# Performance work log

Hardware: AMD Instinct MI355X
Metric: run time of the kernel (lower is better)

The kernel has to match this reference:

```python
import jax, jax.numpy as jnp
import numpy as np

D_IN = 200   # 4 * d_embeddings
H = 64       # hidden_size

def setup_inputs() -> dict:
    key = jax.random.key(0)
    ks = jax.random.split(key, 7)
    B, T = 4096, 128
    s_ih = 1.0 / np.sqrt(H)
    x = jax.random.normal(ks[0], (B, T, D_IN), dtype=jnp.float32)
    W_ih = jax.random.uniform(ks[1], (H, D_IN), minval=-s_ih, maxval=s_ih, dtype=jnp.float32)
    W_hh = jax.random.uniform(ks[2], (H, H), minval=-s_ih, maxval=s_ih, dtype=jnp.float32)
    b_ih = jax.random.uniform(ks[3], (H,), minval=-s_ih, maxval=s_ih, dtype=jnp.float32)
    b_hh = jax.random.uniform(ks[4], (H,), minval=-s_ih, maxval=s_ih, dtype=jnp.float32)
    W_out = jax.random.uniform(ks[5], (1, H), minval=-s_ih, maxval=s_ih, dtype=jnp.float32)
    b_out = jax.random.uniform(ks[6], (1,), minval=-s_ih, maxval=s_ih, dtype=jnp.float32)
    return {"x": x, "W_ih": W_ih, "W_hh": W_hh, "b_ih": b_ih, "b_hh": b_hh,
            "W_out": W_out, "b_out": b_out}

def reference(x, W_ih, W_hh, b_ih, b_hh, W_out, b_out):
    B = x.shape[0]
    # precompute input projection for all timesteps: [B, T, H]
    xp = jnp.einsum('btd,hd->bth', x, W_ih) + b_ih + b_hh
    def step(h, xt):
        h = jnp.tanh(xt + h @ W_hh.T)
        return h, None
    h0 = jnp.zeros((B, H), dtype=x.dtype)
    h_last, _ = jax.lax.scan(step, h0, jnp.swapaxes(xp, 0, 1))  # scan over time
    return jax.nn.sigmoid(h_last @ W_out.T + b_out)  # [B, 1]
```

## Files before the change

### kernel.cpp

```cpp
#include <hip/hip_runtime.h>
#include <hip/hip_bf16.h>


#define TSEQ 128
#define DIN  200
#define HID  64
#define CT   16
#define NCH  (TSEQ/CT)

typedef short bf16x8 __attribute__((ext_vector_type(8)));
typedef float f32x4  __attribute__((ext_vector_type(4)));

__device__ __forceinline__ unsigned short f2bf(float f) {
  __hip_bfloat16 h = __float2bfloat16(f);
  return __builtin_bit_cast(unsigned short, h);
}
__device__ __forceinline__ bf16x8 cvt8(f32x4 a, f32x4 b) {
  bf16x8 r;
#pragma unroll
  for (int i = 0; i < 4; ++i) { r[i] = (short)f2bf(a[i]); r[4 + i] = (short)f2bf(b[i]); }
  return r;
}
__device__ __forceinline__ float tanh_fast(float x) {
  float e = exp2f(x * 2.885390081777927f);
  float r = __builtin_amdgcn_rcpf(1.f + e);
  return __builtin_fmaf(-2.f, r, 1.f);
}

__global__ __launch_bounds__(256, 3) void rnn_fused(
    const float* __restrict__ x,   const float* __restrict__ Wih,
    const float* __restrict__ Whh, const float* __restrict__ bih,
    const float* __restrict__ bhh, const float* __restrict__ Wout,
    const float* __restrict__ bout, float* __restrict__ out)
{
  __shared__ unsigned short wihL[28][64][8];
  __shared__ unsigned short hb[4][2][80];

  const int tid  = threadIdx.x;
  const int w    = tid >> 6;
  const int lane = tid & 63;
  const int m    = lane & 15;
  const int g    = lane >> 4;
  const int row  = blockIdx.x * 4 + w;

  const float* xl = x + ((size_t)row * TSEQ + m) * DIN;

  f32x4 px[7][2];
  auto LOADC = [&](int c) {
    const float* p = xl + (size_t)c * (CT * DIN);
#pragma unroll
    for (int ks = 0; ks < 6; ++ks) {
      const int d = ks * 32 + g * 8;
      px[ks][0] = *reinterpret_cast<const f32x4*>(p + d);
      px[ks][1] = *reinterpret_cast<const f32x4*>(p + d + 4);
    }
    px[6][0] = *reinterpret_cast<const f32x4*>(p + 192);
    px[6][1] = *reinterpret_cast<const f32x4*>(p + 196);
  };
  LOADC(0);

  for (int f = w; f < 28; f += 4) {
    const int nt = f / 7, ks = f % 7;
    const int d  = ks * 32 + g * 8;
    bf16x8 v = (bf16x8)0;
    if (d + 8 <= DIN) {
      const float* wr = Wih + (size_t)(nt * 16 + m) * DIN + d;
      v = cvt8(*reinterpret_cast<const f32x4*>(wr), *reinterpret_cast<const f32x4*>(wr + 4));
    }
    *reinterpret_cast<bf16x8*>(&wihL[f][lane][0]) = v;
  }

  bf16x8 whhf[4][2];
#pragma unroll
  for (int nt = 0; nt < 4; ++nt)
#pragma unroll
    for (int hf = 0; hf < 2; ++hf) {
      const float* wr = Whh + (size_t)(nt * 16 + m) * HID + hf * 32 + g * 8;
      whhf[nt][hf] = cvt8(*reinterpret_cast<const f32x4*>(wr),
                          *reinterpret_cast<const f32x4*>(wr + 4));
    }
  float biasv[4], woutv[4];
#pragma unroll
  for (int nt = 0; nt < 4; ++nt) {
    biasv[nt] = bih[nt * 16 + m] + bhh[nt * 16 + m];
    woutv[nt] = Wout[nt * 16 + m];
  }
  const float bout0 = bout[0];

  hb[w][0][lane] = 0;
  hb[w][1][lane] = 0;
  __syncthreads();

  float vfin[4] = {0.f, 0.f, 0.f, 0.f};

  for (int c = 0; c < NCH; ++c) {
    bf16x8 afr[7];
#pragma unroll
    for (int ks = 0; ks < 6; ++ks) afr[ks] = cvt8(px[ks][0], px[ks][1]);
    afr[6] = (g == 0) ? cvt8(px[6][0], px[6][1]) : (bf16x8)0;

    f32x4 acc[4];
#pragma unroll
    for (int nt = 0; nt < 4; ++nt) acc[nt] = (f32x4)(biasv[nt]);
#pragma unroll
    for (int ks = 0; ks < 7; ++ks) {
#pragma unroll
      for (int nt = 0; nt < 4; ++nt) {
        bf16x8 bv = *reinterpret_cast<const bf16x8*>(&wihL[nt * 7 + ks][lane][0]);
        acc[nt] = __builtin_amdgcn_mfma_f32_16x16x32_bf16(afr[ks], bv, acc[nt], 0, 0, 0);
      }
    }

    if (c + 1 < NCH) LOADC(c + 1);

#pragma unroll
    for (int s = 0; s < CT; ++s) {
      const int rb = s & 1, pb = rb ^ 1;
      asm volatile("" ::: "memory");
      bf16x8 ha0 = *reinterpret_cast<const bf16x8*>(&hb[w][pb][g * 8]);
      bf16x8 ha1 = *reinterpret_cast<const bf16x8*>(&hb[w][pb][32 + g * 8]);
      f32x4 racc[4];
#pragma unroll
      for (int nt = 0; nt < 4; ++nt)
        racc[nt] = __builtin_amdgcn_mfma_f32_16x16x32_bf16(ha0, whhf[nt][0], acc[nt], 0, 0, 0);
#pragma unroll
      for (int nt = 0; nt < 4; ++nt)
        racc[nt] = __builtin_amdgcn_mfma_f32_16x16x32_bf16(ha1, whhf[nt][1], racc[nt], 0, 0, 0);
      if (g == (s >> 2)) {
#pragma unroll
        for (int nt = 0; nt < 4; ++nt) {
          const float v = tanh_fast(racc[nt][s & 3]);
          hb[w][rb][nt * 16 + m] = f2bf(v);
          if (s == CT - 1) vfin[nt] = v;
        }
      }
      asm volatile("" ::: "memory");
    }
  }

  float sred = vfin[0] * woutv[0] + vfin[1] * woutv[1]
             + vfin[2] * woutv[2] + vfin[3] * woutv[3];
  sred += __shfl_xor(sred, 1, 64);
  sred += __shfl_xor(sred, 2, 64);
  sred += __shfl_xor(sred, 4, 64);
  sred += __shfl_xor(sred, 8, 64);
  if (lane == 48)
    out[row] = __builtin_amdgcn_rcpf(1.f + exp2f(-(sred + bout0) * 1.4426950408889634f));
}

extern "C" void kernel_launch(void* const* d_in, const int* in_sizes, int n_in,
                              void* d_out, int out_size, void* d_ws, size_t ws_size,
                              hipStream_t stream) {
  const float* x    = (const float*)d_in[0];
  const float* Wih  = (const float*)d_in[1];
  const float* Whh  = (const float*)d_in[2];
  const float* bih  = (const float*)d_in[3];
  const float* bhh  = (const float*)d_in[4];
  const float* Wout = (const float*)d_in[5];
  const float* bout = (const float*)d_in[6];
  float* out = (float*)d_out;

  const int B = in_sizes[0] / (TSEQ * DIN);
  rnn_fused<<<dim3(B / 4), dim3(256), 0, stream>>>(x, Wih, Whh, bih, bhh, Wout, bout, out);
}
```

Baseline: 117.1 us.

## Split x prefetch into two halves to cut registers and raise occupancy to 4

Launch bounds go from 3 to 4 waves per SIMD. To fit the tighter register budget, the full-chunk x prefetch register array is split in two. The first four k-slices are prefetched one chunk ahead, while the last three are loaded at the start of the current chunk. Wout and bout are now read at the end of the kernel instead of being held in registers. More resident waves should hide latency better, but half of the x loads are no longer overlapped with the recurrence, and spills can happen if the budget is still exceeded.

```diff
diff --git a/kernel.cpp b/kernel.cpp
--- a/kernel.cpp
+++ b/kernel.cpp
@@ -27,7 +27,7 @@
   return __builtin_fmaf(-2.f, r, 1.f);
 }
 
-__global__ __launch_bounds__(256, 3) void rnn_fused(
+__global__ __launch_bounds__(256, 4) void rnn_fused(
     const float* __restrict__ x,   const float* __restrict__ Wih,
     const float* __restrict__ Whh, const float* __restrict__ bih,
     const float* __restrict__ bhh, const float* __restrict__ Wout,
@@ -45,19 +45,28 @@
 
   const float* xl = x + ((size_t)row * TSEQ + m) * DIN;
 
-  f32x4 px[7][2];
-  auto LOADC = [&](int c) {
+  f32x4 pA[4][2], pB[3][2];
+  auto LOADA = [&](int c) {
     const float* p = xl + (size_t)c * (CT * DIN);
 #pragma unroll
-    for (int ks = 0; ks < 6; ++ks) {
+    for (int ks = 0; ks < 4; ++ks) {
       const int d = ks * 32 + g * 8;
-      px[ks][0] = *reinterpret_cast<const f32x4*>(p + d);
-      px[ks][1] = *reinterpret_cast<const f32x4*>(p + d + 4);
+      pA[ks][0] = *reinterpret_cast<const f32x4*>(p + d);
+      pA[ks][1] = *reinterpret_cast<const f32x4*>(p + d + 4);
     }
-    px[6][0] = *reinterpret_cast<const f32x4*>(p + 192);
-    px[6][1] = *reinterpret_cast<const f32x4*>(p + 196);
   };
-  LOADC(0);
+  auto LOADB = [&](int c) {
+    const float* p = xl + (size_t)c * (CT * DIN);
+#pragma unroll
+    for (int ks = 4; ks < 6; ++ks) {
+      const int d = ks * 32 + g * 8;
+      pB[ks - 4][0] = *reinterpret_cast<const f32x4*>(p + d);
+      pB[ks - 4][1] = *reinterpret_cast<const f32x4*>(p + d + 4);
+    }
+    pB[2][0] = *reinterpret_cast<const f32x4*>(p + 192);
+    pB[2][1] = *reinterpret_cast<const f32x4*>(p + 196);
+  };
+  LOADA(0);
 
   for (int f = w; f < 28; f += 4) {
     const int nt = f / 7, ks = f % 7;
@@ -79,13 +88,9 @@
       whhf[nt][hf] = cvt8(*reinterpret_cast<const f32x4*>(wr),
                           *reinterpret_cast<const f32x4*>(wr + 4));
     }
-  float biasv[4], woutv[4];
+  float biasv[4];
 #pragma unroll
-  for (int nt = 0; nt < 4; ++nt) {
-    biasv[nt] = bih[nt * 16 + m] + bhh[nt * 16 + m];
-    woutv[nt] = Wout[nt * 16 + m];
-  }
-  const float bout0 = bout[0];
+  for (int nt = 0; nt < 4; ++nt) biasv[nt] = bih[nt * 16 + m] + bhh[nt * 16 + m];
 
   hb[w][0][lane] = 0;
   hb[w][1][lane] = 0;
@@ -94,24 +99,31 @@
   float vfin[4] = {0.f, 0.f, 0.f, 0.f};
 
   for (int c = 0; c < NCH; ++c) {
-    bf16x8 afr[7];
-#pragma unroll
-    for (int ks = 0; ks < 6; ++ks) afr[ks] = cvt8(px[ks][0], px[ks][1]);
-    afr[6] = (g == 0) ? cvt8(px[6][0], px[6][1]) : (bf16x8)0;
+    LOADB(c);
 
     f32x4 acc[4];
 #pragma unroll
     for (int nt = 0; nt < 4; ++nt) acc[nt] = (f32x4)(biasv[nt]);
 #pragma unroll
-    for (int ks = 0; ks < 7; ++ks) {
+    for (int ks = 0; ks < 4; ++ks) {
+      const bf16x8 a = cvt8(pA[ks][0], pA[ks][1]);
 #pragma unroll
       for (int nt = 0; nt < 4; ++nt) {
         bf16x8 bv = *reinterpret_cast<const bf16x8*>(&wihL[nt * 7 + ks][lane][0]);
-        acc[nt] = __builtin_amdgcn_mfma_f32_16x16x32_bf16(afr[ks], bv, acc[nt], 0, 0, 0);
+        acc[nt] = __builtin_amdgcn_mfma_f32_16x16x32_bf16(a, bv, acc[nt], 0, 0, 0);
       }
     }
-
-    if (c + 1 < NCH) LOADC(c + 1);
+    if (c + 1 < NCH) LOADA(c + 1);
+#pragma unroll
+    for (int ks = 4; ks < 7; ++ks) {
+      const bf16x8 a = (ks < 6) ? cvt8(pB[ks - 4][0], pB[ks - 4][1])
+                                : ((g == 0) ? cvt8(pB[2][0], pB[2][1]) : (bf16x8)0);
+#pragma unroll
+      for (int nt = 0; nt < 4; ++nt) {
+        bf16x8 bv = *reinterpret_cast<const bf16x8*>(&wihL[nt * 7 + ks][lane][0]);
+        acc[nt] = __builtin_amdgcn_mfma_f32_16x16x32_bf16(a, bv, acc[nt], 0, 0, 0);
+      }
+    }
 
 #pragma unroll
     for (int s = 0; s < CT; ++s) {
@@ -138,14 +150,14 @@
     }
   }
 
-  float sred = vfin[0] * woutv[0] + vfin[1] * woutv[1]
-             + vfin[2] * woutv[2] + vfin[3] * woutv[3];
+  float sred = vfin[0] * Wout[m]      + vfin[1] * Wout[16 + m]
+             + vfin[2] * Wout[32 + m] + vfin[3] * Wout[48 + m];
   sred += __shfl_xor(sred, 1, 64);
   sred += __shfl_xor(sred, 2, 64);
   sred += __shfl_xor(sred, 4, 64);
   sred += __shfl_xor(sred, 8, 64);
   if (lane == 48)
-    out[row] = __builtin_amdgcn_rcpf(1.f + exp2f(-(sred + bout0) * 1.4426950408889634f));
+    out[row] = __builtin_amdgcn_rcpf(1.f + exp2f(-(sred + bout[0]) * 1.4426950408889634f));
 }
 
 extern "C" void kernel_launch(void* const* d_in, const int* in_sizes, int n_in,
```

New measurement: 157.3 us (median of 2 runs). 34.3% more time.
